# Kernel tuning notes

Hardware: AMD Instinct MI355X
Metric: run time of the kernel (lower is better)

Reference implementation:

```python
import jax, jax.numpy as jnp
import numpy as np

N = 100000   # nodes
E = 1600000  # edges (avg degree 16)
D = 64       # in_channels
OUT = 64     # out_channels


def setup_inputs() -> dict:
    key = jax.random.key(0)
    k1, k2, k3, k4, k5 = jax.random.split(key, 5)
    x = jax.random.normal(k1, (N, D), jnp.float32)
    edge_index = jax.random.randint(k2, (2, E), 0, N, dtype=jnp.int32)
    x0 = jax.random.normal(k3, (N, D), jnp.float32)
    W_weight = jax.random.normal(k4, (OUT, D), jnp.float32) * (1.0 / np.sqrt(D))
    W_bias = jax.random.normal(k5, (OUT,), jnp.float32) * 0.01
    return {"x": x, "edge_index": edge_index, "x0": x0,
            "W_weight": W_weight, "W_bias": W_bias}


def reference(x, edge_index, x0, W_bias, W_weight):
    n = x.shape[0]
    # gcn_norm with add_self_loops=True (PyG default), improved=False
    self_loops = jnp.arange(n, dtype=edge_index.dtype)
    row = jnp.concatenate([edge_index[0], self_loops])  # source nodes
    col = jnp.concatenate([edge_index[1], self_loops])  # target nodes
    w = jnp.ones(row.shape[0], dtype=x.dtype)
    deg = jax.ops.segment_sum(w, col, num_segments=n)   # in-degree (+1 self loop)
    deg_inv_sqrt = jnp.where(deg > 0, jax.lax.rsqrt(jnp.maximum(deg, 1e-12)), 0.0)
    norm = deg_inv_sqrt[row] * deg_inv_sqrt[col]        # [E+N]
    # SpMM: adj_t = SparseTensor(row=col, col=row) -> out[c] = sum_e norm_e * x[row_e]
    agg = jax.ops.segment_sum(x[row] * norm[:, None], col, num_segments=n)  # [N, D]
    # use_init=False, use_weight=True -> trailing Linear
    return agg @ W_weight.T + W_bias
```

## Files before the change

### kernel.cpp

```cpp
#include <hip/hip_runtime.h>


#define NBMAX 400
#define CAP   5120

typedef short bf16x8 __attribute__((ext_vector_type(8)));
typedef float f32x4  __attribute__((ext_vector_type(4)));

__device__ inline float bflo(unsigned u) { return __uint_as_float(u << 16); }
__device__ inline float bfhi(unsigned u) { return __uint_as_float(u & 0xFFFF0000u); }
__device__ inline unsigned short f2bf(float f) {
    unsigned u = __float_as_uint(f);
    u += 0x7FFFu + ((u >> 16) & 1u);
    return (unsigned short)(u >> 16);
}

__global__ void k_initcur(int* __restrict__ gcur, int NB) {
    int b = threadIdx.x;
    if (b < NB) gcur[b] = b * CAP;
}

__global__ __launch_bounds__(256) void k_bin(const int* __restrict__ row,
                                             const int* __restrict__ col,
                                             int* __restrict__ gcur,
                                             unsigned int* __restrict__ ebuf, int E) {
    __shared__ unsigned int   sorted4[4096];
    __shared__ unsigned short sbkt[4096];
    __shared__ int h[NBMAX], hstart[NBMAX], hcur[NBMAX], gof[NBMAX];
    int t = threadIdx.x;
    int base = blockIdx.x * 4096;
    int total = min(4096, E - base);

    int rr[16], cc[16];
    #pragma unroll
    for (int i = 0; i < 4; ++i) {
        int e0 = (t + i * 256) * 4;
        if (e0 + 3 < total) {
            int4 r4 = *(const int4*)(row + base + e0);
            int4 c4 = *(const int4*)(col + base + e0);
            rr[i*4+0]=r4.x; rr[i*4+1]=r4.y; rr[i*4+2]=r4.z; rr[i*4+3]=r4.w;
            cc[i*4+0]=c4.x; cc[i*4+1]=c4.y; cc[i*4+2]=c4.z; cc[i*4+3]=c4.w;
        } else {
            #pragma unroll
            for (int j = 0; j < 4; ++j) {
                int e = e0 + j;
                if (e < total) { rr[i*4+j] = row[base+e]; cc[i*4+j] = col[base+e]; }
                else cc[i*4+j] = -1;
            }
        }
    }
    for (int b = t; b < NBMAX; b += 256) h[b] = 0;
    __syncthreads();
    #pragma unroll
    for (int i = 0; i < 16; ++i)
        if (cc[i] >= 0) atomicAdd(&h[cc[i] >> 8], 1);
    __syncthreads();
    if (t < 64) {
        int lo = t * 7;
        int loc[7]; int s = 0;
        #pragma unroll
        for (int i = 0; i < 7; ++i) {
            loc[i] = s;
            int idx = lo + i;
            s += (idx < NBMAX) ? h[idx] : 0;
        }
        int incl = s;
        for (int off = 1; off < 64; off <<= 1) {
            int v = __shfl_up(incl, off);
            if (t >= off) incl += v;
        }
        int ex = incl - s;
        #pragma unroll
        for (int i = 0; i < 7; ++i) {
            int idx = lo + i;
            if (idx < NBMAX) hstart[idx] = ex + loc[i];
        }
    }
    __syncthreads();
    for (int b = t; b < NBMAX; b += 256) hcur[b] = hstart[b];
    __syncthreads();
    #pragma unroll
    for (int i = 0; i < 16; ++i) {
        if (cc[i] >= 0) {
            int b = cc[i] >> 8;
            int rank = atomicAdd(&hcur[b], 1);
            sorted4[rank] = (unsigned)rr[i] | ((unsigned)(cc[i] & 255) << 24);
            sbkt[rank] = (unsigned short)b;
        }
    }
    for (int b = t; b < NBMAX; b += 256) {
        int m = h[b];
        gof[b] = m ? atomicAdd(&gcur[b], m) : 0;
    }
    __syncthreads();
    for (int i = t; i < total; i += 256) {
        int b = sbkt[i];
        ebuf[gof[b] + (i - hstart[b])] = sorted4[i];
    }
}

__global__ __launch_bounds__(256) void k_sort(const unsigned int* __restrict__ ebuf,
                                              const int* __restrict__ gcur,
                                              int* __restrict__ srcs,
                                              int2* __restrict__ rowse,
                                              float* __restrict__ dinv, int n) {
    __shared__ int h[256], hc[256], wsum[4];
    __shared__ int sbuf[CAP];
    int b = blockIdx.x, t = threadIdx.x;
    int s0 = b * CAP;
    int count = min(gcur[b] - s0, CAP);

    h[t] = 0;
    __syncthreads();
    uint4 u[5];
    #pragma unroll
    for (int i = 0; i < 5; ++i) {
        int e0 = (t + i * 256) * 4;
        if (e0 + 3 < count) {
            u[i] = *(const uint4*)(ebuf + s0 + e0);
            atomicAdd(&h[u[i].x >> 24], 1);
            atomicAdd(&h[u[i].y >> 24], 1);
            atomicAdd(&h[u[i].z >> 24], 1);
            atomicAdd(&h[u[i].w >> 24], 1);
        }
    }
    unsigned tailp = 0; bool tailv = false;
    {
        int i = (count & ~3) + t;
        if (i < count) { tailp = ebuf[s0 + i]; tailv = true; atomicAdd(&h[tailp >> 24], 1); }
    }
    __syncthreads();
    int v = h[t];
    int lane = t & 63, wid = t >> 6;
    int incl = v;
    #pragma unroll
    for (int off = 1; off < 64; off <<= 1) {
        int uu = __shfl_up(incl, off);
        if (lane >= off) incl += uu;
    }
    if (lane == 63) wsum[wid] = incl;
    __syncthreads();
    int add = 0;
    for (int w = 0; w < wid; ++w) add += wsum[w];
    int ex = incl - v + add;
    hc[t] = ex;
    int c = b * 256 + t;
    if (c < n) {
        dinv[c] = rsqrtf((float)(v + 1));
        rowse[c] = make_int2(s0 + ex, s0 + ex + v);
    }
    __syncthreads();
    #pragma unroll
    for (int i = 0; i < 5; ++i) {
        int e0 = (t + i * 256) * 4;
        if (e0 + 3 < count) {
            int r;
            r = atomicAdd(&hc[u[i].x >> 24], 1); sbuf[r] = (int)(u[i].x & 0x1FFFFu);
            r = atomicAdd(&hc[u[i].y >> 24], 1); sbuf[r] = (int)(u[i].y & 0x1FFFFu);
            r = atomicAdd(&hc[u[i].z >> 24], 1); sbuf[r] = (int)(u[i].z & 0x1FFFFu);
            r = atomicAdd(&hc[u[i].w >> 24], 1); sbuf[r] = (int)(u[i].w & 0x1FFFFu);
        }
    }
    if (tailv) {
        int r = atomicAdd(&hc[tailp >> 24], 1);
        sbuf[r] = (int)(tailp & 0x1FFFFu);
    }
    __syncthreads();
    for (int i = t; i < count; i += 256) srcs[s0 + i] = sbuf[i];
}

__global__ __launch_bounds__(256) void k_gemm(const float* __restrict__ x,
                                              const float* __restrict__ W,
                                              const float* __restrict__ dinv,
                                              unsigned short* __restrict__ yb, int n) {
    __shared__ __align__(16) unsigned short xs[64][72];
    __shared__ __align__(16) unsigned short Wb[64][72];
    int t = threadIdx.x;
    long long total = (long long)n * 64;
    long long xbase = (long long)blockIdx.x * 4096;
    #pragma unroll
    for (int i = 0; i < 4; ++i) {
        int idx = t + i * 256;
        int r = idx >> 4, c4 = (idx & 15) << 2;
        long long g = xbase + (long long)idx * 4;
        float4 v;
        if (g + 3 < total) v = *(const float4*)(x + g);
        else {
            v.x = (g + 0 < total) ? x[g + 0] : 0.f;
            v.y = (g + 1 < total) ? x[g + 1] : 0.f;
            v.z = (g + 2 < total) ? x[g + 2] : 0.f;
            v.w = (g + 3 < total) ? x[g + 3] : 0.f;
        }
        ushort4 o; o.x = f2bf(v.x); o.y = f2bf(v.y); o.z = f2bf(v.z); o.w = f2bf(v.w);
        *(ushort4*)&xs[r][c4] = o;
        float4 wv = *(const float4*)(W + idx * 4);
        ushort4 wo; wo.x = f2bf(wv.x); wo.y = f2bf(wv.y); wo.z = f2bf(wv.z); wo.w = f2bf(wv.w);
        *(ushort4*)&Wb[r][c4] = wo;
    }
    __syncthreads();
    int lane = t & 63, wid = t >> 6;
    int m  = wid * 16 + (lane & 15);
    int kg = (lane >> 4) * 8;
    bf16x8 a0 = *(bf16x8*)&xs[m][kg];
    bf16x8 a1 = *(bf16x8*)&xs[m][32 + kg];
    int bn = lane & 15;
    f32x4 acc0 = {0.f,0.f,0.f,0.f}, acc1 = acc0, acc2 = acc0, acc3 = acc0;
    {
        bf16x8 b0 = *(bf16x8*)&Wb[bn][kg], b1 = *(bf16x8*)&Wb[bn][32 + kg];
        acc0 = __builtin_amdgcn_mfma_f32_16x16x32_bf16(a0, b0, acc0, 0, 0, 0);
        acc0 = __builtin_amdgcn_mfma_f32_16x16x32_bf16(a1, b1, acc0, 0, 0, 0);
    }
    {
        bf16x8 b0 = *(bf16x8*)&Wb[bn + 16][kg], b1 = *(bf16x8*)&Wb[bn + 16][32 + kg];
        acc1 = __builtin_amdgcn_mfma_f32_16x16x32_bf16(a0, b0, acc1, 0, 0, 0);
        acc1 = __builtin_amdgcn_mfma_f32_16x16x32_bf16(a1, b1, acc1, 0, 0, 0);
    }
    {
        bf16x8 b0 = *(bf16x8*)&Wb[bn + 32][kg], b1 = *(bf16x8*)&Wb[bn + 32][32 + kg];
        acc2 = __builtin_amdgcn_mfma_f32_16x16x32_bf16(a0, b0, acc2, 0, 0, 0);
        acc2 = __builtin_amdgcn_mfma_f32_16x16x32_bf16(a1, b1, acc2, 0, 0, 0);
    }
    {
        bf16x8 b0 = *(bf16x8*)&Wb[bn + 48][kg], b1 = *(bf16x8*)&Wb[bn + 48][32 + kg];
        acc3 = __builtin_amdgcn_mfma_f32_16x16x32_bf16(a0, b0, acc3, 0, 0, 0);
        acc3 = __builtin_amdgcn_mfma_f32_16x16x32_bf16(a1, b1, acc3, 0, 0, 0);
    }
    int rbase = blockIdx.x * 64 + wid * 16 + (lane >> 4) * 4;
    #pragma unroll
    for (int i = 0; i < 4; ++i) {
        int r = rbase + i;
        if (r < n) {
            float dv = dinv[r];
            long long ro = (long long)r * 64 + (lane & 15);
            yb[ro +  0] = f2bf(dv * acc0[i]);
            yb[ro + 16] = f2bf(dv * acc1[i]);
            yb[ro + 32] = f2bf(dv * acc2[i]);
            yb[ro + 48] = f2bf(dv * acc3[i]);
        }
    }
}

__global__ __launch_bounds__(256) void k_gather(const int2* __restrict__ rowse,
                                                const int* __restrict__ srcs,
                                                const unsigned short* __restrict__ yb,
                                                const float* __restrict__ dinv,
                                                const float* __restrict__ bias,
                                                float* __restrict__ out, int n) {
    int c = blockIdx.x * 4 + (threadIdx.x >> 6);
    if (c >= n) return;
    int lane = threadIdx.x & 63;
    int g = lane >> 4;
    int q = lane & 15;
    int2 se = rowse[c];
    int start = se.x, end = se.y;

    float a0 = 0.f, a1 = 0.f, a2 = 0.f, a3 = 0.f;
    for (int base = start; base < end; base += 64) {
        int sv = srcs[base + lane];
        int m = min(end - base, 64);
        for (int it = 0; it < m; it += 4) {
            int idx = it + g;
            int src = __shfl(sv, idx);
            bool valid = idx < m;
            int sa = valid ? src : c;
            float2 v = *(const float2*)(yb + (long long)sa * 64 + (q << 2));
            if (valid) {
                unsigned u0 = __float_as_uint(v.x), u1 = __float_as_uint(v.y);
                a0 += bflo(u0); a1 += bfhi(u0);
                a2 += bflo(u1); a3 += bfhi(u1);
            }
        }
    }
    #pragma unroll
    for (int off = 16; off < 64; off <<= 1) {
        a0 += __shfl_xor(a0, off);
        a1 += __shfl_xor(a1, off);
        a2 += __shfl_xor(a2, off);
        a3 += __shfl_xor(a3, off);
    }
    if (g == 0) {
        float2 v = *(const float2*)(yb + (long long)c * 64 + (q << 2));
        unsigned u0 = __float_as_uint(v.x), u1 = __float_as_uint(v.y);
        a0 += bflo(u0); a1 += bfhi(u0);
        a2 += bflo(u1); a3 += bfhi(u1);
        float dc = dinv[c];
        float4 bv = *(const float4*)(bias + (q << 2));
        *(float4*)(out + (long long)c * 64 + (q << 2)) =
            make_float4(dc * a0 + bv.x, dc * a1 + bv.y,
                        dc * a2 + bv.z, dc * a3 + bv.w);
    }
}

extern "C" void kernel_launch(void* const* d_in, const int* in_sizes, int n_in,
                              void* d_out, int out_size, void* d_ws, size_t ws_size,
                              hipStream_t stream) {
    const float* x    = (const float*)d_in[0];
    const int*   ei   = (const int*)d_in[1];
    const float* W    = (const float*)d_in[3];
    const float* bias = (const float*)d_in[4];
    float* out = (float*)d_out;

    int n = in_sizes[0] / 64;
    int E = in_sizes[1] / 2;
    const int* row = ei;
    const int* col = ei + E;

    int NB = (n + 255) / 256;

    char* ws = (char*)d_ws;
    size_t off = 0;
    auto alloc = [&](size_t bytes) { char* p = ws + off; off += (bytes + 15) & ~size_t(15); return p; };
    int*            gcur  = (int*)  alloc((size_t)NB * 4);
    float*          dinv  = (float*)alloc((size_t)n * 4);
    int2*           rowse = (int2*) alloc((size_t)n * 8);
    unsigned short* yb    = (unsigned short*)alloc((size_t)n * 64 * 2);
    unsigned int*   ebuf  = (unsigned int*)alloc((size_t)NB * CAP * 4);
    int*            srcs  = (int*)  alloc(((size_t)NB * CAP + 64) * 4);

    int nbE = (E + 4095) / 4096;

    k_initcur<<<1, 512, 0, stream>>>(gcur, NB);
    k_bin    <<<nbE, 256, 0, stream>>>(row, col, gcur, ebuf, E);
    k_sort   <<<NB, 256, 0, stream>>>(ebuf, gcur, srcs, rowse, dinv, n);
    k_gemm   <<<(n + 63) / 64, 256, 0, stream>>>(x, W, dinv, yb, n);
    k_gather <<<(n + 3) / 4, 256, 0, stream>>>(rowse, srcs, yb, dinv, bias, out, n);
}
```

Before: 182.2 us.

## Fuse per-bucket sort into aggregation kernel and compute degrees via global atomics

Drops the separate k_sort kernel and the srcs/rowse/dinv arrays. The in-bucket counting sort now runs in shared memory inside a new 1024-thread k_aggr kernel, which then aggregates neighbor rows straight from the sorted shared buffer. Degrees come from a new k_deg kernel that does global atomics on col and also initializes gcur, and dinv is recomputed from those counts wherever it is needed. This removes one kernel launch and the global round trip of the sorted indices. In exchange it adds an E-wide atomic pass and changes the gather so that 16 lanes walk each node's edges serially, which is less parallel than the old wave-per-node scheme.

New measurement: 236.5 us. +29.8%, slower.

```diff
diff --git a/kernel.cpp b/kernel.cpp
--- a/kernel.cpp
+++ b/kernel.cpp
@@ -15,9 +15,20 @@
     return (unsigned short)(u >> 16);
 }
 
-__global__ void k_initcur(int* __restrict__ gcur, int NB) {
-    int b = threadIdx.x;
-    if (b < NB) gcur[b] = b * CAP;
+__global__ __launch_bounds__(256) void k_deg(const int* __restrict__ col,
+                                             int* __restrict__ cnt,
+                                             int* __restrict__ gcur, int E, int NB) {
+    if (blockIdx.x == 0)
+        for (int b = threadIdx.x; b < NB; b += 256) gcur[b] = b * CAP;
+    int i4 = (blockIdx.x * 256 + threadIdx.x) * 4;
+    if (i4 + 3 < E) {
+        int4 c = *(const int4*)(col + i4);
+        atomicAdd(&cnt[c.x], 1); atomicAdd(&cnt[c.y], 1);
+        atomicAdd(&cnt[c.z], 1); atomicAdd(&cnt[c.w], 1);
+    } else {
+        int lim = min(i4 + 4, E);
+        for (int j = i4; j < lim; ++j) atomicAdd(&cnt[col[j]], 1);
+    }
 }
 
 __global__ __launch_bounds__(256) void k_bin(const int* __restrict__ row,
@@ -99,79 +110,9 @@
     }
 }
 
-__global__ __launch_bounds__(256) void k_sort(const unsigned int* __restrict__ ebuf,
-                                              const int* __restrict__ gcur,
-                                              int* __restrict__ srcs,
-                                              int2* __restrict__ rowse,
-                                              float* __restrict__ dinv, int n) {
-    __shared__ int h[256], hc[256], wsum[4];
-    __shared__ int sbuf[CAP];
-    int b = blockIdx.x, t = threadIdx.x;
-    int s0 = b * CAP;
-    int count = min(gcur[b] - s0, CAP);
-
-    h[t] = 0;
-    __syncthreads();
-    uint4 u[5];
-    #pragma unroll
-    for (int i = 0; i < 5; ++i) {
-        int e0 = (t + i * 256) * 4;
-        if (e0 + 3 < count) {
-            u[i] = *(const uint4*)(ebuf + s0 + e0);
-            atomicAdd(&h[u[i].x >> 24], 1);
-            atomicAdd(&h[u[i].y >> 24], 1);
-            atomicAdd(&h[u[i].z >> 24], 1);
-            atomicAdd(&h[u[i].w >> 24], 1);
-        }
-    }
-    unsigned tailp = 0; bool tailv = false;
-    {
-        int i = (count & ~3) + t;
-        if (i < count) { tailp = ebuf[s0 + i]; tailv = true; atomicAdd(&h[tailp >> 24], 1); }
-    }
-    __syncthreads();
-    int v = h[t];
-    int lane = t & 63, wid = t >> 6;
-    int incl = v;
-    #pragma unroll
-    for (int off = 1; off < 64; off <<= 1) {
-        int uu = __shfl_up(incl, off);
-        if (lane >= off) incl += uu;
-    }
-    if (lane == 63) wsum[wid] = incl;
-    __syncthreads();
-    int add = 0;
-    for (int w = 0; w < wid; ++w) add += wsum[w];
-    int ex = incl - v + add;
-    hc[t] = ex;
-    int c = b * 256 + t;
-    if (c < n) {
-        dinv[c] = rsqrtf((float)(v + 1));
-        rowse[c] = make_int2(s0 + ex, s0 + ex + v);
-    }
-    __syncthreads();
-    #pragma unroll
-    for (int i = 0; i < 5; ++i) {
-        int e0 = (t + i * 256) * 4;
-        if (e0 + 3 < count) {
-            int r;
-            r = atomicAdd(&hc[u[i].x >> 24], 1); sbuf[r] = (int)(u[i].x & 0x1FFFFu);
-            r = atomicAdd(&hc[u[i].y >> 24], 1); sbuf[r] = (int)(u[i].y & 0x1FFFFu);
-            r = atomicAdd(&hc[u[i].z >> 24], 1); sbuf[r] = (int)(u[i].z & 0x1FFFFu);
-            r = atomicAdd(&hc[u[i].w >> 24], 1); sbuf[r] = (int)(u[i].w & 0x1FFFFu);
-        }
-    }
-    if (tailv) {
-        int r = atomicAdd(&hc[tailp >> 24], 1);
-        sbuf[r] = (int)(tailp & 0x1FFFFu);
-    }
-    __syncthreads();
-    for (int i = t; i < count; i += 256) srcs[s0 + i] = sbuf[i];
-}
-
 __global__ __launch_bounds__(256) void k_gemm(const float* __restrict__ x,
                                               const float* __restrict__ W,
-                                              const float* __restrict__ dinv,
+                                              const int* __restrict__ cnt,
                                               unsigned short* __restrict__ yb, int n) {
     __shared__ __align__(16) unsigned short xs[64][72];
     __shared__ __align__(16) unsigned short Wb[64][72];
@@ -230,7 +171,7 @@
     for (int i = 0; i < 4; ++i) {
         int r = rbase + i;
         if (r < n) {
-            float dv = dinv[r];
+            float dv = rsqrtf((float)(cnt[r] + 1));
             long long ro = (long long)r * 64 + (lane & 15);
             yb[ro +  0] = f2bf(dv * acc0[i]);
             yb[ro + 16] = f2bf(dv * acc1[i]);
@@ -240,50 +181,91 @@
     }
 }
 
-__global__ __launch_bounds__(256) void k_gather(const int2* __restrict__ rowse,
-                                                const int* __restrict__ srcs,
-                                                const unsigned short* __restrict__ yb,
-                                                const float* __restrict__ dinv,
-                                                const float* __restrict__ bias,
-                                                float* __restrict__ out, int n) {
-    int c = blockIdx.x * 4 + (threadIdx.x >> 6);
-    if (c >= n) return;
-    int lane = threadIdx.x & 63;
-    int g = lane >> 4;
-    int q = lane & 15;
-    int2 se = rowse[c];
-    int start = se.x, end = se.y;
-
-    float a0 = 0.f, a1 = 0.f, a2 = 0.f, a3 = 0.f;
-    for (int base = start; base < end; base += 64) {
-        int sv = srcs[base + lane];
-        int m = min(end - base, 64);
-        for (int it = 0; it < m; it += 4) {
-            int idx = it + g;
-            int src = __shfl(sv, idx);
-            bool valid = idx < m;
-            int sa = valid ? src : c;
-            float2 v = *(const float2*)(yb + (long long)sa * 64 + (q << 2));
-            if (valid) {
+__global__ __launch_bounds__(1024) void k_aggr(const unsigned int* __restrict__ ebuf,
+                                               const int* __restrict__ gcur,
+                                               const int* __restrict__ cnt,
+                                               const unsigned short* __restrict__ yb,
+                                               const float* __restrict__ bias,
+                                               float* __restrict__ out, int n) {
+    __shared__ int h[256], hstart[256], hc[256], wsum[4];
+    __shared__ int sbuf[CAP];
+    int b = blockIdx.x, t = threadIdx.x;
+    int s0 = b * CAP;
+    int count = min(gcur[b] - s0, CAP);
+
+    if (t < 256) h[t] = 0;
+    __syncthreads();
+    unsigned rec[5];
+    #pragma unroll
+    for (int k = 0; k < 5; ++k) {
+        int i = t + k * 1024;
+        if (i < count) {
+            unsigned p = ebuf[s0 + i];
+            rec[k] = p;
+            atomicAdd(&h[p >> 24], 1);
+        }
+    }
+    __syncthreads();
+    if (t < 256) {
+        int v = h[t];
+        int lane = t & 63, wid = t >> 6;
+        int incl = v;
+        #pragma unroll
+        for (int off = 1; off < 64; off <<= 1) {
+            int u = __shfl_up(incl, off);
+            if (lane >= off) incl += u;
+        }
+        hstart[t] = incl;
+        if (lane == 63) wsum[wid] = incl;
+    }
+    __syncthreads();
+    if (t < 256) {
+        int wid = t >> 6;
+        int add = 0;
+        for (int w = 0; w < wid; ++w) add += wsum[w];
+        int ex = hstart[t] - h[t] + add;
+        hstart[t] = ex;
+        hc[t] = ex;
+    }
+    __syncthreads();
+    #pragma unroll
+    for (int k = 0; k < 5; ++k) {
+        int i = t + k * 1024;
+        if (i < count) {
+            unsigned p = rec[k];
+            int r = atomicAdd(&hc[p >> 24], 1);
+            sbuf[r] = (int)(p & 0x1FFFFu);
+        }
+    }
+    __syncthreads();
+
+    int lane = t & 63, w = t >> 6;
+    int g = lane >> 4, q = lane & 15;
+    #pragma unroll
+    for (int r = 0; r < 4; ++r) {
+        int cl = r * 64 + w * 4 + g;
+        int c = b * 256 + cl;
+        if (c >= n) continue;
+        int start = hstart[cl], len = h[cl];
+        float a0 = 0.f, a1 = 0.f, a2 = 0.f, a3 = 0.f;
+        if (len > 0) {
+            int sc = sbuf[start];
+            for (int i = 0; i < len; ++i) {
+                int sn = (i + 1 < len) ? sbuf[start + i + 1] : 0;
+                float2 v = *(const float2*)(yb + (long long)sc * 64 + (q << 2));
                 unsigned u0 = __float_as_uint(v.x), u1 = __float_as_uint(v.y);
                 a0 += bflo(u0); a1 += bfhi(u0);
                 a2 += bflo(u1); a3 += bfhi(u1);
+                sc = sn;
             }
         }
-    }
-    #pragma unroll
-    for (int off = 16; off < 64; off <<= 1) {
-        a0 += __shfl_xor(a0, off);
-        a1 += __shfl_xor(a1, off);
-        a2 += __shfl_xor(a2, off);
-        a3 += __shfl_xor(a3, off);
-    }
-    if (g == 0) {
-        float2 v = *(const float2*)(yb + (long long)c * 64 + (q << 2));
-        unsigned u0 = __float_as_uint(v.x), u1 = __float_as_uint(v.y);
-        a0 += bflo(u0); a1 += bfhi(u0);
-        a2 += bflo(u1); a3 += bfhi(u1);
-        float dc = dinv[c];
+        {
+            float2 v = *(const float2*)(yb + (long long)c * 64 + (q << 2));
+            unsigned u0 = __float_as_uint(v.x), u1 = __float_as_uint(v.y);
+            a0 += bflo(u0); a1 += bfhi(u0);
+            a2 += bflo(u1); a3 += bfhi(u1);
+        }
+        float dc = rsqrtf((float)(cnt[c] + 1));
         float4 bv = *(const float4*)(bias + (q << 2));
         *(float4*)(out + (long long)c * 64 + (q << 2)) =
             make_float4(dc * a0 + bv.x, dc * a1 + bv.y,
@@ -310,18 +292,16 @@
     char* ws = (char*)d_ws;
     size_t off = 0;
     auto alloc = [&](size_t bytes) { char* p = ws + off; off += (bytes + 15) & ~size_t(15); return p; };
-    int*            gcur  = (int*)  alloc((size_t)NB * 4);
-    float*          dinv  = (float*)alloc((size_t)n * 4);
-    int2*           rowse = (int2*) alloc((size_t)n * 8);
-    unsigned short* yb    = (unsigned short*)alloc((size_t)n * 64 * 2);
-    unsigned int*   ebuf  = (unsigned int*)alloc((size_t)NB * CAP * 4);
-    int*            srcs  = (int*)  alloc(((size_t)NB * CAP + 64) * 4);
+    int*            cnt  = (int*)  alloc((size_t)n * 4);
+    int*            gcur = (int*)  alloc((size_t)NB * 4);
+    unsigned short* yb   = (unsigned short*)alloc((size_t)n * 64 * 2);
+    unsigned int*   ebuf = (unsigned int*)alloc((size_t)NB * CAP * 4);
 
     int nbE = (E + 4095) / 4096;
 
-    k_initcur<<<1, 512, 0, stream>>>(gcur, NB);
-    k_bin    <<<nbE, 256, 0, stream>>>(row, col, gcur, ebuf, E);
-    k_sort   <<<NB, 256, 0, stream>>>(ebuf, gcur, srcs, rowse, dinv, n);
-    k_gemm   <<<(n + 63) / 64, 256, 0, stream>>>(x, W, dinv, yb, n);
-    k_gather <<<(n + 3) / 4, 256, 0, stream>>>(rowse, srcs, yb, dinv, bias, out, n);
-}
+    hipMemsetAsync(cnt, 0, (size_t)n * 4, stream);
+    k_deg <<<(E / 4 + 255) / 256, 256, 0, stream>>>(col, cnt, gcur, E, NB);
+    k_bin <<<nbE, 256, 0, stream>>>(row, col, gcur, ebuf, E);
+    k_gemm<<<(n + 63) / 64, 256, 0, stream>>>(x, W, cnt, yb, n);
+    k_aggr<<<NB, 1024, 0, stream>>>(ebuf, gcur, cnt, yb, bias, out, n);
+}
```
